# Kernel tuning notes

Hardware: AMD Instinct MI355X
Metric: run time of the kernel (lower is better)

## Reference

```python
import jax, jax.numpy as jnp
import numpy as np

EMBED_DIM = 1024
NUM_HEADS = 16
NUM_KV_HEADS = 4
HEAD_DIM = EMBED_DIM // NUM_HEADS  # 64
N_GROUP = NUM_HEADS // NUM_KV_HEADS  # 4
KV_DIM = NUM_KV_HEADS * HEAD_DIM  # 256


def setup_inputs() -> dict:
    key = jax.random.key(0)
    ks = jax.random.split(key, 9)
    B, T = 1, 4096
    s_in = 1.0 / np.sqrt(EMBED_DIM)
    inp = {
        "x": jax.random.normal(ks[0], (B, T, EMBED_DIM), dtype=jnp.float32),
        "Wq": jax.random.normal(ks[1], (EMBED_DIM, EMBED_DIM), dtype=jnp.float32) * s_in,
        "bq": jnp.zeros((EMBED_DIM,), dtype=jnp.float32),
        "Wk": jax.random.normal(ks[2], (KV_DIM, EMBED_DIM), dtype=jnp.float32) * s_in,
        "bk": jnp.zeros((KV_DIM,), dtype=jnp.float32),
        "Wv": jax.random.normal(ks[3], (KV_DIM, EMBED_DIM), dtype=jnp.float32) * s_in,
        "bv": jnp.zeros((KV_DIM,), dtype=jnp.float32),
        "Wo": jax.random.normal(ks[4], (EMBED_DIM, EMBED_DIM), dtype=jnp.float32) * s_in,
        "bo": jnp.zeros((EMBED_DIM,), dtype=jnp.float32),
    }
    return inp


def reference(x, Wq, bq, Wk, bk, Wv, bv, Wo, bo):
    B, T, C = x.shape
    scale = HEAD_DIM ** -0.5
    # projections (torch Linear: x @ W.T + b)
    Q = x @ Wq.T + bq  # [B,T,C]
    K = x @ Wk.T + bk  # [B,T,KV_DIM]
    V = x @ Wv.T + bv
    Q = Q.reshape(B, T, NUM_HEADS, HEAD_DIM).transpose(0, 2, 1, 3)      # [B,H,T,D]
    K = K.reshape(B, T, NUM_KV_HEADS, HEAD_DIM).transpose(0, 2, 1, 3)   # [B,Hkv,T,D]
    V = V.reshape(B, T, NUM_KV_HEADS, HEAD_DIM).transpose(0, 2, 1, 3)
    new_kv = (K, V)
    # GQA: group Q heads over KV heads instead of materializing repeated K/V
    Qg = Q.reshape(B, NUM_KV_HEADS, N_GROUP, T, HEAD_DIM)  # head h uses kv head h//N_GROUP
    scores = jnp.einsum('bkgqd,bkvd->bkgqv', Qg, K) * scale  # [B,Hkv,G,T,T]
    weights = jax.nn.softmax(scores, axis=-1)
    out = jnp.einsum('bkgqv,bkvd->bkgqd', weights, V)  # [B,Hkv,G,T,D]
    out = out.reshape(B, NUM_HEADS, T, HEAD_DIM).transpose(0, 2, 1, 3).reshape(B, T, C)
    output = out @ Wo.T + bo
    return (output, new_kv)
```

## Files before the change

kernel.cpp:

```cpp
#include <hip/hip_runtime.h>
#include <hip/hip_bf16.h>
#include <math.h>

typedef unsigned short u16;
typedef unsigned int u32;
typedef __bf16 bf16;
typedef __bf16 bf16x8 __attribute__((ext_vector_type(8)));
typedef float f32x4 __attribute__((ext_vector_type(4)));
typedef float f32x16 __attribute__((ext_vector_type(16)));
typedef u16 u16x2 __attribute__((ext_vector_type(2)));
typedef u16 u16x4 __attribute__((ext_vector_type(4)));
typedef u16 u16x8 __attribute__((ext_vector_type(8)));
typedef u32 u32x4 __attribute__((ext_vector_type(4)));

#define QSCALE 0.1803368801111204f

static __device__ __forceinline__ u16 f2b(float f) {
  return __builtin_bit_cast(u16, (bf16)f);
}
static __device__ __forceinline__ u32 pack2(float a, float b) {
  u16x2 p = { f2b(a), f2b(b) };
  return __builtin_bit_cast(u32, p);
}

static __device__ __forceinline__ f32x4 mfma16(u16x8 a, u16x8 b, f32x4 c) {
  return __builtin_amdgcn_mfma_f32_16x16x32_bf16(
      __builtin_bit_cast(bf16x8, a), __builtin_bit_cast(bf16x8, b), c, 0, 0, 0);
}
static __device__ __forceinline__ f32x16 mfma32(u16x8 a, u16x8 b, f32x16 c) {
  return __builtin_amdgcn_mfma_f32_32x32x16_bf16(
      __builtin_bit_cast(bf16x8, a), __builtin_bit_cast(bf16x8, b), c, 0, 0, 0);
}

static __device__ __forceinline__ void pl32swap(u32& a, u32& b) {
  asm("v_permlane32_swap_b32 %0, %1" : "+v"(a), "+v"(b));
}

static __device__ __forceinline__ void glds16(const u16* g, u16* l) {
  __builtin_amdgcn_global_load_lds(
      (const __attribute__((address_space(1))) void*)g,
      (__attribute__((address_space(3))) void*)l, 16, 0, 0);
}

#define WAIT_VM0() asm volatile("s_waitcnt vmcnt(0)" ::: "memory")

static __device__ __forceinline__ u16x8 ldsrd(const u16* base, int row, int slot) {
  return *(const u16x8*)(base + row * 64 + ((slot ^ (row & 7)) * 8));
}

__global__ void cast_f32_bf16(const float* __restrict__ src, u16* __restrict__ dst, int n4) {
  int i = blockIdx.x * blockDim.x + threadIdx.x;
  int stride = gridDim.x * blockDim.x;
  for (; i < n4; i += stride) {
    f32x4 v = ((const f32x4*)src)[i];
    u16x4 o;
#pragma unroll
    for (int r = 0; r < 4; r++) o[r] = f2b(v[r]);
    ((u16x4*)dst)[i] = o;
  }
}

__global__ void cast_weights(const float* __restrict__ Wq, const float* __restrict__ Wk,
                             const float* __restrict__ Wv, const float* __restrict__ Wo,
                             u16* __restrict__ wqkv, u16* __restrict__ wo16) {
  int i = blockIdx.x * blockDim.x + threadIdx.x;
  int stride = gridDim.x * blockDim.x;
  for (; i < 655360; i += stride) {
    const float* src; u16* dst; int j;
    if (i < 262144)      { src = Wq; dst = wqkv;           j = i; }
    else if (i < 327680) { src = Wk; dst = wqkv + 1048576; j = i - 262144; }
    else if (i < 393216) { src = Wv; dst = wqkv + 1310720; j = i - 327680; }
    else                 { src = Wo; dst = wo16;           j = i - 393216; }
    f32x4 v = ((const f32x4*)src)[j];
    u16x4 o;
#pragma unroll
    for (int r = 0; r < 4; r++) o[r] = f2b(v[r]);
    ((u16x4*)dst)[j] = o;
  }
}

__global__ void transpose_v(const u16* __restrict__ vb, u16* __restrict__ vt) {
  __shared__ u16 T[64][72];
  const int kh = blockIdx.y;
  const int t0 = blockIdx.x * 64;
  const int tid = threadIdx.x;
  const int r = tid >> 2, c0 = (tid & 3) * 16;
  const u16* src = vb + ((size_t)kh * 4096 + t0 + r) * 64 + c0;
  *(u16x8*)&T[r][c0] = *(const u16x8*)src;
  *(u16x8*)&T[r][c0 + 8] = *(const u16x8*)(src + 8);
  __syncthreads();
  const int d = tid >> 2, j0 = (tid & 3) * 16;
  u16x8 o0, o1;
#pragma unroll
  for (int j = 0; j < 8; j++) o0[j] = T[j0 + j][d];
#pragma unroll
  for (int j = 0; j < 8; j++) o1[j] = T[j0 + 8 + j][d];
  u16* dst = vt + ((size_t)kh * 64 + d) * 4096 + t0 + j0;
  *(u16x8*)dst = o0;
  *(u16x8*)(dst + 8) = o1;
}

template<int MODE>
__global__ __launch_bounds__(256, 2) void gemm_bt(
    const u16* __restrict__ A, const u16* __restrict__ B,
    const float* __restrict__ b0, const float* __restrict__ b1,
    const float* __restrict__ b2,
    float* __restrict__ outF,
    u16* __restrict__ qs, u16* __restrict__ kb, u16* __restrict__ vb,
    int K) {
  __shared__ u16 As[2][128 * 64];
  __shared__ u16 Bs[2][128 * 64];
  const int t = threadIdx.x, w = t >> 6, l = t & 63;
  const int c = l & 15, g = l >> 4;
  const int n0 = blockIdx.x * 128, m0 = blockIdx.y * 128;
  const int nrow0 = (w >> 1) * 64, mrow0 = (w & 1) * 64;
  const int srow = l >> 3, sslot = l & 7;

  f32x4 acc[4][4];
  f32x4 z = {0.f, 0.f, 0.f, 0.f};
#pragma unroll
  for (int i = 0; i < 4; i++)
#pragma unroll
    for (int j = 0; j < 4; j++) acc[i][j] = z;

#pragma unroll
  for (int p = 0; p < 4; p++) {
    int row = p * 32 + w * 8 + srow;
    int ss = sslot ^ (row & 7);
    glds16(A + (size_t)(m0 + row) * K + ss * 8, &As[0][p * 2048 + w * 512]);
    glds16(B + (size_t)(n0 + row) * K + ss * 8, &Bs[0][p * 2048 + w * 512]);
  }
  WAIT_VM0();
  __builtin_amdgcn_s_barrier();

  const int NS = K >> 6;
  for (int st = 0; st < NS; ++st) {
    const int cur = st & 1;
    if (st + 1 < NS) {
      int kt = (st + 1) * 64;
#pragma unroll
      for (int p = 0; p < 4; p++) {
        int row = p * 32 + w * 8 + srow;
        int ss = sslot ^ (row & 7);
        glds16(A + (size_t)(m0 + row) * K + kt + ss * 8, &As[cur ^ 1][p * 2048 + w * 512]);
        glds16(B + (size_t)(n0 + row) * K + kt + ss * 8, &Bs[cur ^ 1][p * 2048 + w * 512]);
      }
    }
    __builtin_amdgcn_s_setprio(1);
#pragma unroll
    for (int ks = 0; ks < 2; ks++) {
      u16x8 af[4], bf[4];
#pragma unroll
      for (int nj = 0; nj < 4; nj++) af[nj] = ldsrd(Bs[cur], nrow0 + 16 * nj + c, g + 4 * ks);
#pragma unroll
      for (int mi = 0; mi < 4; mi++) bf[mi] = ldsrd(As[cur], mrow0 + 16 * mi + c, g + 4 * ks);
#pragma unroll
      for (int nj = 0; nj < 4; nj++)
#pragma unroll
        for (int mi = 0; mi < 4; mi++) acc[nj][mi] = mfma16(af[nj], bf[mi], acc[nj][mi]);
    }
    __builtin_amdgcn_s_setprio(0);
    WAIT_VM0();
    __builtin_amdgcn_s_barrier();
  }

#pragma unroll
  for (int nj = 0; nj < 4; nj++) {
#pragma unroll
    for (int mi = 0; mi < 4; mi++) {
      int n = n0 + nrow0 + 16 * nj + 4 * g;
      int m = m0 + mrow0 + 16 * mi + c;
      f32x4 v = acc[nj][mi];
      if (MODE == 1) {
        f32x4 bb = *(const f32x4*)(b0 + n);
        v += bb;
        *(f32x4*)(outF + (size_t)m * 1024 + n) = v;
      } else {
        if (n < 1024) {
          f32x4 bb = *(const f32x4*)(b0 + n);
          v += bb;
          u16x4 q;
#pragma unroll
          for (int r = 0; r < 4; r++) q[r] = f2b(v[r] * QSCALE);
          *(u16x4*)(qs + (size_t)m * 1024 + n) = q;
        } else if (n < 1280) {
          int nn = n - 1024, khh = nn >> 6, d = nn & 63;
          f32x4 bb = *(const f32x4*)(b1 + nn);
          v += bb;
          *(f32x4*)(outF + (size_t)4194304 + (size_t)(khh * 4096 + m) * 64 + d) = v;
          u16x4 kq;
#pragma unroll
          for (int r = 0; r < 4; r++) kq[r] = f2b(v[r]);
          *(u16x4*)(kb + (size_t)(khh * 4096 + m) * 64 + d) = kq;
        } else {
          int nn = n - 1280, khh = nn >> 6, d = nn & 63;
          f32x4 bb = *(const f32x4*)(b2 + nn);
          v += bb;
          *(f32x4*)(outF + (size_t)5242880 + (size_t)(khh * 4096 + m) * 64 + d) = v;
          u16x4 vq;
#pragma unroll
          for (int r = 0; r < 4; r++) vq[r] = f2b(v[r]);
          *(u16x4*)(vb + (size_t)(khh * 4096 + m) * 64 + d) = vq;
        }
      }
    }
  }
}

__global__ __launch_bounds__(256, 2) void attn_fwd(
    const u16* __restrict__ qs, const u16* __restrict__ kb,
    const u16* __restrict__ vt, u16* __restrict__ att) {
  __shared__ u16 Ks[2][64 * 64];
  __shared__ u16 Vs[2][64 * 64];
  const int h = blockIdx.y, kh = h >> 2;
  const int q0 = blockIdx.x * 128;
  const int t = threadIdx.x, w = t >> 6, l = t & 63;
  const int ql = l & 31, hh = l >> 5;
  const int srow = l >> 3, sslot = l & 7;

  const u16* kbase = kb + (size_t)kh * 262144;
  const u16* vbase = vt + (size_t)kh * 262144;

  u16x8 qf[4];
#pragma unroll
  for (int ks = 0; ks < 4; ks++)
    qf[ks] = *(const u16x8*)(qs + (size_t)(q0 + w * 32 + ql) * 1024 + h * 64 + ks * 16 + hh * 8);

  u16x8 onesf;
#pragma unroll
  for (int j = 0; j < 8; j++) onesf[j] = 0x3F80;

  f32x16 o0v, o1v, lacc;
#pragma unroll
  for (int i = 0; i < 16; i++) { o0v[i] = 0.f; o1v[i] = 0.f; lacc[i] = 0.f; }
  float m_r = -INFINITY;

#pragma unroll
  for (int p = 0; p < 2; p++) {
    int row = p * 32 + w * 8 + srow;
    int ss = sslot ^ (row & 7);
    glds16(kbase + (size_t)row * 64 + ss * 8, &Ks[0][p * 2048 + w * 512]);
    glds16(vbase + (size_t)row * 4096 + ss * 8, &Vs[0][p * 2048 + w * 512]);
  }
  WAIT_VM0();
  __builtin_amdgcn_s_barrier();

  for (int tt = 0; tt < 64; ++tt) {
    const int cur = tt & 1;
    const u16* KsC = Ks[cur];
    const u16* VsC = Vs[cur];
    if (tt < 63) {
      int kv = (tt + 1) * 64;
#pragma unroll
      for (int p = 0; p < 2; p++) {
        int row = p * 32 + w * 8 + srow;
        int ss = sslot ^ (row & 7);
        glds16(kbase + (size_t)(kv + row) * 64 + ss * 8, &Ks[cur ^ 1][p * 2048 + w * 512]);
        glds16(vbase + (size_t)row * 4096 + kv + ss * 8, &Vs[cur ^ 1][p * 2048 + w * 512]);
      }
    }

    f32x16 sA, sB;
#pragma unroll
    for (int i = 0; i < 16; i++) { sA[i] = 0.f; sB[i] = 0.f; }
    __builtin_amdgcn_s_setprio(1);
#pragma unroll
    for (int ks = 0; ks < 4; ks++) {
      u16x8 kf0 = ldsrd(KsC, ql, 2 * ks + hh);
      u16x8 kf1 = ldsrd(KsC, 32 + ql, 2 * ks + hh);
      sA = mfma32(kf0, qf[ks], sA);
      sB = mfma32(kf1, qf[ks], sB);
    }
    __builtin_amdgcn_s_setprio(0);

    float mx[16];
#pragma unroll
    for (int i = 0; i < 16; i++) mx[i] = fmaxf(sA[i], sB[i]);
#pragma unroll
    for (int stp = 8; stp > 0; stp >>= 1)
#pragma unroll
      for (int i = 0; i < stp; i++) mx[i] = fmaxf(mx[i], mx[i + stp]);
    float pm = fmaxf(mx[0], __shfl_xor(mx[0], 32));

    if (!__all(pm - m_r <= 8.0f)) {
      float mn = fmaxf(m_r, pm);
      float fac = __builtin_amdgcn_exp2f(m_r - mn);
      m_r = mn;
      o0v *= fac; o1v *= fac; lacc *= fac;
    }

    u32 pw0[8], pw1[8];
#pragma unroll
    for (int i = 0; i < 8; i++) {
      pw0[i] = pack2(__builtin_amdgcn_exp2f(sA[2 * i] - m_r),
                     __builtin_amdgcn_exp2f(sA[2 * i + 1] - m_r));
      pw1[i] = pack2(__builtin_amdgcn_exp2f(sB[2 * i] - m_r),
                     __builtin_amdgcn_exp2f(sB[2 * i + 1] - m_r));
    }

    __builtin_amdgcn_s_setprio(1);
#pragma unroll
    for (int t4 = 0; t4 < 4; t4++) {
      u32 a0, a1, b0, b1;
      if (t4 == 0)      { a0 = pw0[0]; a1 = pw0[1]; b0 = pw0[2]; b1 = pw0[3]; }
      else if (t4 == 1) { a0 = pw0[4]; a1 = pw0[5]; b0 = pw0[6]; b1 = pw0[7]; }
      else if (t4 == 2) { a0 = pw1[0]; a1 = pw1[1]; b0 = pw1[2]; b1 = pw1[3]; }
      else              { a0 = pw1[4]; a1 = pw1[5]; b0 = pw1[6]; b1 = pw1[7]; }
      pl32swap(a0, b0);
      pl32swap(a1, b1);
      u32x4 pv4 = {a0, a1, b0, b1};
      u16x8 pf = __builtin_bit_cast(u16x8, pv4);
      u16x8 vf0 = ldsrd(VsC, ql, 2 * t4 + hh);
      u16x8 vf1 = ldsrd(VsC, 32 + ql, 2 * t4 + hh);
      o0v = mfma32(vf0, pf, o0v);
      o1v = mfma32(vf1, pf, o1v);
      lacc = mfma32(onesf, pf, lacc);
    }
    __builtin_amdgcn_s_setprio(0);

    WAIT_VM0();
    __builtin_amdgcn_s_barrier();
  }

  float inv = 1.f / lacc[0];
  const size_t obase = (size_t)(q0 + w * 32 + ql) * 1024 + h * 64;
#pragma unroll
  for (int dj = 0; dj < 2; dj++)
#pragma unroll
    for (int rq = 0; rq < 4; rq++) {
      u16x4 ov;
#pragma unroll
      for (int r = 0; r < 4; r++)
        ov[r] = f2b((dj ? o1v[rq * 4 + r] : o0v[rq * 4 + r]) * inv);
      *(u16x4*)(att + obase + dj * 32 + rq * 8 + hh * 4) = ov;
    }
}

extern "C" void kernel_launch(void* const* d_in, const int* in_sizes, int n_in,
                              void* d_out, int out_size, void* d_ws, size_t ws_size,
                              hipStream_t stream) {
  const float* x  = (const float*)d_in[0];
  const float* Wq = (const float*)d_in[1];
  const float* bq = (const float*)d_in[2];
  const float* Wk = (const float*)d_in[3];
  const float* bk = (const float*)d_in[4];
  const float* Wv = (const float*)d_in[5];
  const float* bv = (const float*)d_in[6];
  const float* Wo = (const float*)d_in[7];
  const float* bo = (const float*)d_in[8];
  float* out = (float*)d_out;
  char* ws = (char*)d_ws;

  u16* X16  = (u16*)(ws);
  u16* WQKV = (u16*)(ws + 8388608);
  u16* VT   = (u16*)(ws + 8388608);
  u16* WO16 = (u16*)(ws + 11534336);
  u16* QS   = (u16*)(ws + 13631488);
  u16* KB   = (u16*)(ws + 22020096);
  u16* VB   = (u16*)(ws + 24117248);
  u16* ATT  = X16;

  cast_f32_bf16<<<1024, 256, 0, stream>>>(x, X16, 4096 * 1024 / 4);
  cast_weights<<<512, 256, 0, stream>>>(Wq, Wk, Wv, Wo, WQKV, WO16);

  gemm_bt<0><<<dim3(12, 32), 256, 0, stream>>>(X16, WQKV, bq, bk, bv, out, QS, KB, VB, 1024);
  transpose_v<<<dim3(64, 4), 256, 0, stream>>>(VB, VT);
  attn_fwd<<<dim3(32, 16), 256, 0, stream>>>(QS, KB, VT, ATT);
  gemm_bt<1><<<dim3(8, 32), 256, 0, stream>>>(ATT, WO16, bo, nullptr, nullptr, out,
                                              nullptr, nullptr, nullptr, 1024);
}
```

Baseline: 241.2 us.

## Split attention over KV halves with merge kernel, fuse casts, widen swizzle

Result: no change. 243.9 us (+1.1%).

```diff
diff --git a/kernel.cpp b/kernel.cpp
--- a/kernel.cpp
+++ b/kernel.cpp
@@ -18,6 +18,9 @@
 static __device__ __forceinline__ u16 f2b(float f) {
   return __builtin_bit_cast(u16, (bf16)f);
 }
+static __device__ __forceinline__ float b2f(u16 u) {
+  return __builtin_bit_cast(float, (u32)u << 16);
+}
 static __device__ __forceinline__ u32 pack2(float a, float b) {
   u16x2 p = { f2b(a), f2b(b) };
   return __builtin_bit_cast(u32, p);
@@ -44,33 +47,27 @@
 
 #define WAIT_VM0() asm volatile("s_waitcnt vmcnt(0)" ::: "memory")
 
+static __device__ __forceinline__ int swz(int row) {
+  return (row & 7) ^ ((row >> 3) & 7);
+}
 static __device__ __forceinline__ u16x8 ldsrd(const u16* base, int row, int slot) {
-  return *(const u16x8*)(base + row * 64 + ((slot ^ (row & 7)) * 8));
-}
-
-__global__ void cast_f32_bf16(const float* __restrict__ src, u16* __restrict__ dst, int n4) {
+  return *(const u16x8*)(base + row * 64 + ((slot ^ swz(row)) * 8));
+}
+
+__global__ void cast_all(const float* __restrict__ x,
+                         const float* __restrict__ Wq, const float* __restrict__ Wk,
+                         const float* __restrict__ Wv, const float* __restrict__ Wo,
+                         u16* __restrict__ x16, u16* __restrict__ wqkv,
+                         u16* __restrict__ wo16) {
   int i = blockIdx.x * blockDim.x + threadIdx.x;
   int stride = gridDim.x * blockDim.x;
-  for (; i < n4; i += stride) {
-    f32x4 v = ((const f32x4*)src)[i];
-    u16x4 o;
-#pragma unroll
-    for (int r = 0; r < 4; r++) o[r] = f2b(v[r]);
-    ((u16x4*)dst)[i] = o;
-  }
-}
-
-__global__ void cast_weights(const float* __restrict__ Wq, const float* __restrict__ Wk,
-                             const float* __restrict__ Wv, const float* __restrict__ Wo,
-                             u16* __restrict__ wqkv, u16* __restrict__ wo16) {
-  int i = blockIdx.x * blockDim.x + threadIdx.x;
-  int stride = gridDim.x * blockDim.x;
-  for (; i < 655360; i += stride) {
+  for (; i < 1703936; i += stride) {
     const float* src; u16* dst; int j;
-    if (i < 262144)      { src = Wq; dst = wqkv;           j = i; }
-    else if (i < 327680) { src = Wk; dst = wqkv + 1048576; j = i - 262144; }
-    else if (i < 393216) { src = Wv; dst = wqkv + 1310720; j = i - 327680; }
-    else                 { src = Wo; dst = wo16;           j = i - 393216; }
+    if (i < 1048576)      { src = x;  dst = x16;            j = i; }
+    else if (i < 1310720) { src = Wq; dst = wqkv;           j = i - 1048576; }
+    else if (i < 1376256) { src = Wk; dst = wqkv + 1048576; j = i - 1310720; }
+    else if (i < 1441792) { src = Wv; dst = wqkv + 1310720; j = i - 1376256; }
+    else                  { src = Wo; dst = wo16;           j = i - 1441792; }
     f32x4 v = ((const f32x4*)src)[j];
     u16x4 o;
 #pragma unroll
@@ -126,7 +123,7 @@
 #pragma unroll
   for (int p = 0; p < 4; p++) {
     int row = p * 32 + w * 8 + srow;
-    int ss = sslot ^ (row & 7);
+    int ss = sslot ^ swz(row);
     glds16(A + (size_t)(m0 + row) * K + ss * 8, &As[0][p * 2048 + w * 512]);
     glds16(B + (size_t)(n0 + row) * K + ss * 8, &Bs[0][p * 2048 + w * 512]);
   }
@@ -141,7 +138,7 @@
 #pragma unroll
       for (int p = 0; p < 4; p++) {
         int row = p * 32 + w * 8 + srow;
-        int ss = sslot ^ (row & 7);
+        int ss = sslot ^ swz(row);
         glds16(A + (size_t)(m0 + row) * K + kt + ss * 8, &As[cur ^ 1][p * 2048 + w * 512]);
         glds16(B + (size_t)(n0 + row) * K + kt + ss * 8, &Bs[cur ^ 1][p * 2048 + w * 512]);
       }
@@ -207,19 +204,21 @@
   }
 }
 
-__global__ __launch_bounds__(256, 2) void attn_fwd(
+__global__ __launch_bounds__(256, 4) void attn_fwd(
     const u16* __restrict__ qs, const u16* __restrict__ kb,
-    const u16* __restrict__ vt, u16* __restrict__ att) {
+    const u16* __restrict__ vt, u16* __restrict__ op0, u16* __restrict__ op1,
+    float* __restrict__ ml, int ntiles) {
   __shared__ u16 Ks[2][64 * 64];
   __shared__ u16 Vs[2][64 * 64];
-  const int h = blockIdx.y, kh = h >> 2;
+  const int h = blockIdx.y, kh = h >> 2, zz = blockIdx.z;
   const int q0 = blockIdx.x * 128;
+  const int kv0 = zz * ntiles * 64;
   const int t = threadIdx.x, w = t >> 6, l = t & 63;
   const int ql = l & 31, hh = l >> 5;
   const int srow = l >> 3, sslot = l & 7;
 
-  const u16* kbase = kb + (size_t)kh * 262144;
-  const u16* vbase = vt + (size_t)kh * 262144;
+  const u16* kbase = kb + (size_t)kh * 262144 + (size_t)kv0 * 64;
+  const u16* vbase = vt + (size_t)kh * 262144 + kv0;
 
   u16x8 qf[4];
 #pragma unroll
@@ -238,23 +237,23 @@
 #pragma unroll
   for (int p = 0; p < 2; p++) {
     int row = p * 32 + w * 8 + srow;
-    int ss = sslot ^ (row & 7);
+    int ss = sslot ^ swz(row);
     glds16(kbase + (size_t)row * 64 + ss * 8, &Ks[0][p * 2048 + w * 512]);
     glds16(vbase + (size_t)row * 4096 + ss * 8, &Vs[0][p * 2048 + w * 512]);
   }
   WAIT_VM0();
   __builtin_amdgcn_s_barrier();
 
-  for (int tt = 0; tt < 64; ++tt) {
+  for (int tt = 0; tt < ntiles; ++tt) {
     const int cur = tt & 1;
     const u16* KsC = Ks[cur];
     const u16* VsC = Vs[cur];
-    if (tt < 63) {
+    if (tt + 1 < ntiles) {
       int kv = (tt + 1) * 64;
 #pragma unroll
       for (int p = 0; p < 2; p++) {
         int row = p * 32 + w * 8 + srow;
-        int ss = sslot ^ (row & 7);
+        int ss = sslot ^ swz(row);
         glds16(kbase + (size_t)(kv + row) * 64 + ss * 8, &Ks[cur ^ 1][p * 2048 + w * 512]);
         glds16(vbase + (size_t)row * 4096 + kv + ss * 8, &Vs[cur ^ 1][p * 2048 + w * 512]);
       }
@@ -322,8 +321,9 @@
     __builtin_amdgcn_s_barrier();
   }
 
-  float inv = 1.f / lacc[0];
-  const size_t obase = (size_t)(q0 + w * 32 + ql) * 1024 + h * 64;
+  u16* dst = zz ? op1 : op0;
+  const int q = q0 + w * 32 + ql;
+  const size_t obase = (size_t)q * 1024 + h * 64;
 #pragma unroll
   for (int dj = 0; dj < 2; dj++)
 #pragma unroll
@@ -331,9 +331,37 @@
       u16x4 ov;
 #pragma unroll
       for (int r = 0; r < 4; r++)
-        ov[r] = f2b((dj ? o1v[rq * 4 + r] : o0v[rq * 4 + r]) * inv);
-      *(u16x4*)(att + obase + dj * 32 + rq * 8 + hh * 4) = ov;
-    }
+        ov[r] = f2b(dj ? o1v[rq * 4 + r] : o0v[rq * 4 + r]);
+      *(u16x4*)(dst + obase + dj * 32 + rq * 8 + hh * 4) = ov;
+    }
+  if (hh == 0)
+    *(float2*)(ml + (((size_t)zz * 16 + h) * 4096 + q) * 2) = make_float2(m_r, lacc[0]);
+}
+
+__global__ void merge_o(u16* __restrict__ op0, const u16* __restrict__ op1,
+                        const float* __restrict__ ml, int nz) {
+  int idx = blockIdx.x * blockDim.x + threadIdx.x;
+  int q = idx >> 7, c8 = idx & 127;
+  int h = c8 >> 3;
+  size_t off = (size_t)q * 1024 + c8 * 8;
+  u16x8 a = *(u16x8*)(op0 + off);
+  const float2 ml0 = *(const float2*)(ml + ((size_t)h * 4096 + q) * 2);
+  u16x8 r;
+  if (nz == 2) {
+    u16x8 b = *(const u16x8*)(op1 + off);
+    const float2 ml1 = *(const float2*)(ml + ((size_t)(16 + h) * 4096 + q) * 2);
+    float m = fmaxf(ml0.x, ml1.x);
+    float e0 = exp2f(ml0.x - m), e1 = exp2f(ml1.x - m);
+    float inv = 1.f / (ml0.y * e0 + ml1.y * e1);
+    e0 *= inv; e1 *= inv;
+#pragma unroll
+    for (int j = 0; j < 8; j++) r[j] = f2b(b2f(a[j]) * e0 + b2f(b[j]) * e1);
+  } else {
+    float inv = 1.f / ml0.y;
+#pragma unroll
+    for (int j = 0; j < 8; j++) r[j] = f2b(b2f(a[j]) * inv);
+  }
+  *(u16x8*)(op0 + off) = r;
 }
 
 extern "C" void kernel_launch(void* const* d_in, const int* in_sizes, int n_in,
@@ -354,18 +382,22 @@
   u16* X16  = (u16*)(ws);
   u16* WQKV = (u16*)(ws + 8388608);
   u16* VT   = (u16*)(ws + 8388608);
+  float* ML = (float*)(ws + 10485760);
   u16* WO16 = (u16*)(ws + 11534336);
   u16* QS   = (u16*)(ws + 13631488);
   u16* KB   = (u16*)(ws + 22020096);
   u16* VB   = (u16*)(ws + 24117248);
+  u16* OP1  = (u16*)(ws + 26214400);
   u16* ATT  = X16;
 
-  cast_f32_bf16<<<1024, 256, 0, stream>>>(x, X16, 4096 * 1024 / 4);
-  cast_weights<<<512, 256, 0, stream>>>(Wq, Wk, Wv, Wo, WQKV, WO16);
+  const int nz = (ws_size >= (size_t)34603008) ? 2 : 1;
+
+  cast_all<<<2048, 256, 0, stream>>>(x, Wq, Wk, Wv, Wo, X16, WQKV, WO16);
 
   gemm_bt<0><<<dim3(12, 32), 256, 0, stream>>>(X16, WQKV, bq, bk, bv, out, QS, KB, VB, 1024);
   transpose_v<<<dim3(64, 4), 256, 0, stream>>>(VB, VT);
-  attn_fwd<<<dim3(32, 16), 256, 0, stream>>>(QS, KB, VT, ATT);
+  attn_fwd<<<dim3(32, 16, nz), 256, 0, stream>>>(QS, KB, VT, ATT, OP1, ML, 64 / nz);
+  merge_o<<<2048, 256, 0, stream>>>(ATT, OP1, ML, nz);
   gemm_bt<1><<<dim3(8, 32), 256, 0, stream>>>(ATT, WO16, bo, nullptr, nullptr, out,
                                               nullptr, nullptr, nullptr, 1024);
 }
```
